# Optimization experiments

Hardware: AMD Instinct MI355X
Metric: run time of the kernel (lower is better)

Reference implementation:

```python
import jax, jax.numpy as jnp
import numpy as np
import math

FREQ = 24        # seasonality period (hours)
GAMMA = 1.0      # Matern-1/2 lengthscale (frozen in the module)
ISO = 1e-4       # global likelihood noise
TASK_NOISE = 1.0 # per-task noise (all set to 1, frozen)


def _matern12(t1, t2, ell):
    # Matern nu=0.5: k(r) = exp(-r/ell)
    return jnp.exp(-jnp.abs(t1[:, None] - t2[None, :]) / ell)


def setup_inputs() -> dict:
    key = jax.random.key(0)
    k1, k2, k3 = jax.random.split(key, 3)
    B, C, pred_len, ctx_freqs, rank = 8, 128, 24, 2, 8
    L = ctx_freqs * pred_len
    x = jax.random.normal(k1, (B, C, L), dtype=jnp.float32)
    V = jax.random.normal(k2, (C, rank), dtype=jnp.float32) * 0.3      # task covar factor
    task_var = jax.random.uniform(k3, (C,), dtype=jnp.float32) + 0.1   # task covar diag
    return {"x": x, "V": V, "task_var": task_var,
            "prediction_length": pred_len, "context_points": pred_len}


def reference(x, V, task_var, prediction_length, context_points):
    B, C, L = x.shape
    F = FREQ
    # t = arange(window_length) * pi / freq, window = context_points + prediction_length
    t = jnp.arange(context_points + prediction_length, dtype=jnp.float32) * (math.pi / F)

    # --- seasonal per-phase mean over the context (torch repeat_interleave semantics) ---
    G = L // F
    loc_phase = x[:, :, :G * F].reshape(B, C, G, F).mean(axis=2)       # [B,C,F]
    loc_ctx = jnp.repeat(loc_phase, G, axis=2)                          # [B,C,G*F]
    rem = L % F
    if rem > 0:
        loc_ctx = jnp.concatenate([loc_ctx, loc_phase[:, :, :rem]], axis=2)
    y_ctx = (x - loc_ctx).transpose(0, 2, 1)                            # [B,L,C]
    Y = y_ctx[:, L - context_points:, :]                                # [B,Lc,C] GP targets

    # --- kernels ---
    t_ctx = t[:context_points]
    t_fut = t[context_points:context_points + prediction_length]
    Kc = _matern12(t_ctx, t_ctx, GAMMA)                                 # [Lc,Lc]
    Kfc = _matern12(t_fut, t_ctx, GAMMA)                                # [Lf,Lc]
    Kff = _matern12(t_fut, t_fut, GAMMA)                                # [Lf,Lf]
    Bt = V @ V.T + jnp.diag(task_var)                                   # task covariance [C,C]
    sigma2 = TASK_NOISE + ISO                                           # isotropic noise

    # --- exact multitask GP posterior via Kronecker eigendecomposition ---
    # (Kc (x) Bt + sigma2 I)^{-1} = (U (x) P) diag(1/(s_i lam_j + sigma2)) (U (x) P)^T
    s, U = jnp.linalg.eigh(Kc)
    lam, P = jnp.linalg.eigh(Bt)
    D = s[:, None] * lam[None, :] + sigma2                               # [Lc,C]
    Yt = jnp.einsum('il,blc,cm->bim', U, Y, P)
    alpha = jnp.einsum('il,blm,cm->bic', U, Yt / D, P)                   # [B,Lc,C]
    mean_f = jnp.einsum('fi,bic,cd->bfd', Kfc, alpha, Bt)                # [B,Lf,C]

    # --- add back future seasonal mean ---
    fc, rf = divmod(prediction_length, F)
    fut_loc = jnp.repeat(loc_phase, fc, axis=2) if fc > 0 else jnp.zeros((B, C, 0), x.dtype)
    if rf > 0:
        fut_loc = jnp.concatenate([fut_loc, loc_phase[:, :, :rf]], axis=2)
    mean_final = mean_f + fut_loc.transpose(0, 2, 1)                     # [B,Lf,C]

    # --- predictive covariance of y_fut (task-interleaved: K_time (x) K_task) ---
    # shared across batch since all kernel/noise hypers are shared
    A = Kfc @ U                                                          # [Lf,Lc]
    Cm = Bt @ P                                                          # [C,C] (= P * lam)
    W = (A[:, None, :, None] * Cm[None, :, None, :]) / jnp.sqrt(D)[None, None]
    Lf = prediction_length
    W = W.reshape(Lf * C, context_points * C)
    prior = jnp.einsum('fg,cd->fcgd', Kff, Bt).reshape(Lf * C, Lf * C)
    cov = prior - W @ W.T + sigma2 * jnp.eye(Lf * C, dtype=x.dtype)      # + likelihood noise
    cov = jnp.broadcast_to(cov, (B, Lf * C, Lf * C))
    return mean_final, cov
```

## Files before the change

### kernel.cpp

```cpp
#include <hip/hip_runtime.h>
#include <math.h>

#define NB 8
#define NC 128
#define NR 8
#define NT 24
#define SIG2 1.0001f

#define OFF_KFC   0
#define OFF_KFF   576
#define OFF_U     1152
#define OFF_S     1728
#define OFF_KU    1752
#define OFF_BT    2328
#define OFF_DVEC  18712
#define OFF_VD    21784
#define OFF_INVM  46360
#define OFF_W     47896
#define OFF_J     72472
#define OFF_N     97048
#define OFF_Y     490264
#define OFF_Z     514840
#define OFF_H2    539416
#define OFF_LOCP  563992


static inline float h_fsign(float a, float b){ return copysignf(fabsf(a), b); }

static float h_slapy2(float x, float y){
  float xa=fabsf(x), ya=fabsf(y);
  float w=fmaxf(xa,ya), z=fminf(xa,ya);
  if (z==0.f) return w;
  float t=z/w;
  return w*sqrtf(1.f+t*t);
}

static void h_slartg(float f, float g, float& c, float& s, float& r){
  const float safmin=1.17549435e-38f;
  const float safmax=1.f/1.17549435e-38f;
  float f1=fabsf(f), g1=fabsf(g);
  if (g==0.f){ c=1.f; s=0.f; r=f; }
  else if (f==0.f){ c=0.f; s=copysignf(1.f,g); r=g1; }
  else {
    float rtmin=sqrtf(safmin);
    float rtmax=sqrtf(safmax*0.5f);
    if (f1>rtmin && f1<rtmax && g1>rtmin && g1<rtmax){
      float d=sqrtf(f*f+g*g);
      c=f1/d;
      r=copysignf(d,f);
      s=g/r;
    } else {
      float u=fminf(safmax, fmaxf(safmin, fmaxf(f1,g1)));
      float fs=f/u, gs=g/u;
      float d=sqrtf(fs*fs+gs*gs);
      c=fabsf(fs)/d;
      r=copysignf(d,f);
      s=gs/r;
      r=r*u;
    }
  }
}

static void h_slaev2(float a, float b, float c, float& rt1, float& rt2, float& cs1, float& sn1){
  float sm=a+c, df=a-c, adf=fabsf(df), tb=b+b, ab=fabsf(tb);
  float acmx, acmn;
  if (fabsf(a)>fabsf(c)){acmx=a;acmn=c;} else {acmx=c;acmn=a;}
  float rt;
  if (adf>ab){ float t=ab/adf; rt=adf*sqrtf(1.f+t*t); }
  else if (adf<ab){ float t=adf/ab; rt=ab*sqrtf(1.f+t*t); }
  else rt=ab*sqrtf(2.f);
  int sgn1;
  if (sm<0.f){ rt1=0.5f*(sm-rt); sgn1=-1; rt2=(acmx/rt1)*acmn-(b/rt1)*b; }
  else if (sm>0.f){ rt1=0.5f*(sm+rt); sgn1=1; rt2=(acmx/rt1)*acmn-(b/rt1)*b; }
  else { rt1=0.5f*rt; rt2=-0.5f*rt; sgn1=1; }
  float cs; int sgn2;
  if (df>=0.f){ cs=df+rt; sgn2=1; } else { cs=df-rt; sgn2=-1; }
  float acs=fabsf(cs);
  if (acs>ab){ float ct=-tb/cs; sn1=1.f/sqrtf(1.f+ct*ct); cs1=ct*sn1; }
  else {
    if (ab==0.f){ cs1=1.f; sn1=0.f; }
    else { float tn=-cs/tb; cs1=1.f/sqrtf(1.f+tn*tn); sn1=tn*cs1; }
  }
  if (sgn1==sgn2){ float tn=cs1; cs1=-sn1; sn1=tn; }
}

static void host_eigh(float* Uout , float* Sout ){
  float A[24][24], Z[24][24], dd[24], ee[24], tauv[24], wcA[24], wsA[24];
  const float h = (float)(3.14159265358979323846/24.0);
  for (int i=0;i<24;i++) for (int j=0;j<24;j++){
    float ti=(float)i*h, tj=(float)j*h;
    A[i][j]=expf(-fabsf(ti-tj));
  }
  for (int i0=0;i0<23;i0++){
    float alpha=A[i0+1][i0];
    float scale=0.f, ssq=1.f;
    for (int r=i0+2;r<24;r++){
      float ax=fabsf(A[r][i0]);
      if (ax!=0.f){
        if (scale<ax){ float t=scale/ax; ssq=1.f+ssq*t*t; scale=ax; }
        else { float t=ax/scale; ssq+=t*t; }
      }
    }
    float xnorm=scale*sqrtf(ssq);
    float taui, beta;
    if (xnorm==0.f){ taui=0.f; beta=alpha; }
    else {
      beta=-h_fsign(h_slapy2(alpha,xnorm), alpha);
      taui=(beta-alpha)/beta;
      float sc=1.f/(alpha-beta);
      for (int r=i0+2;r<24;r++) A[r][i0]*=sc;
    }
    ee[i0]=beta; tauv[i0]=taui;
    A[i0+1][i0]=1.f;
    if (taui!=0.f){
      int m=23-i0;
      float w[24];
      for (int jj=0;jj<m;jj++){
        int j=i0+1+jj;
        float acc=0.f;
        for (int k=i0+1;k<=j;k++) acc+=A[j][k]*A[k][i0];
        for (int k=j+1;k<24;k++)  acc+=A[k][j]*A[k][i0];
        w[jj]=taui*acc;
      }
      float dt=0.f;
      for (int r=0;r<m;r++) dt+=w[r]*A[i0+1+r][i0];
      float al=-0.5f*taui*dt;
      for (int r=0;r<m;r++) w[r]+=al*A[i0+1+r][i0];
      for (int jj=0;jj<m;jj++){
        int j=i0+1+jj;
        float vj=A[j][i0], wj=w[jj];
        for (int k=i0+1;k<=j;k++) A[j][k]-=vj*w[k-(i0+1)]+wj*A[k][i0];
      }
    }
    A[i0+1][i0]=ee[i0]; dd[i0]=A[i0][i0];
  }
  dd[23]=A[23][23];
  for (int i=0;i<24;i++) for (int j=0;j<24;j++) Z[i][j]=(i==j)?1.f:0.f;
  const float LEPS=5.9604645e-08f, EPS2=LEPS*LEPS, SAFMIN=1.17549435e-38f;
  const float SSFMAX=sqrtf(1.f/SAFMIN)/3.f, SSFMIN=sqrtf(SAFMIN)/EPS2;
  const int NMAXIT=720;
  #define D1(i) dd[(i)-1]
  #define E1(i) ee[(i)-1]
  #define WC1(i) wcA[(i)-1]
  #define WS1(i) wsA[(i)-1]
  int l=1,lend=1,lsv=1,lendsv=1,l1=1,jtot=0,iscale=0;
  float anorm=0.f;
  int phase=0;
  for (int guard=0; guard<200000; ++guard){
    if (phase==4) break;
    if (phase==0){
      if (l1>24){ phase=4; continue; }
      if (l1>1) E1(l1-1)=0.f;
      int m=24;
      for (int mm=l1; mm<=23; mm++){
        float tst=fabsf(E1(mm));
        if (tst==0.f){ m=mm; break; }
        if (tst<=(sqrtf(fabsf(D1(mm)))*sqrtf(fabsf(D1(mm+1))))*LEPS){ E1(mm)=0.f; m=mm; break; }
      }
      l=l1; lsv=l; lend=m; lendsv=m; l1=m+1;
      if (lend==l) continue;
      anorm=0.f;
      for (int i=l;i<=lend;i++) anorm=fmaxf(anorm,fabsf(D1(i)));
      for (int i=l;i<=lend-1;i++) anorm=fmaxf(anorm,fabsf(E1(i)));
      iscale=0;
      if (anorm==0.f) continue;
      if (anorm>SSFMAX){ iscale=1; float sc=SSFMAX/anorm; for (int i=l;i<=lend;i++) D1(i)*=sc; for (int i=l;i<lend;i++) E1(i)*=sc; }
      else if (anorm<SSFMIN){ iscale=2; float sc=SSFMIN/anorm; for (int i=l;i<=lend;i++) D1(i)*=sc; for (int i=l;i<lend;i++) E1(i)*=sc; }
      if (fabsf(D1(lend))<fabsf(D1(l))){ lend=lsv; l=lendsv; }
      phase=(lend>l)?1:2;
      continue;
    }
    if (phase==1){
      int m=lend;
      if (l!=lend){
        for (int mm=l;mm<=lend-1;mm++){
          float tst=fabsf(E1(mm)); tst*=tst;
          if (tst<=(EPS2*fabsf(D1(mm)))*fabsf(D1(mm+1))+SAFMIN){ m=mm; break; }
        }
      }
      if (m<lend) E1(m)=0.f;
      float p=D1(l);
      if (m==l){ D1(l)=p; l=l+1; if (l>lend) phase=3; continue; }
      if (m==l+1){
        float rt1,rt2,cc,ssv;
        h_slaev2(D1(l),E1(l),D1(l+1),rt1,rt2,cc,ssv);
        WC1(l)=cc; WS1(l)=ssv;
        D1(l)=rt1; D1(l+1)=rt2; E1(l)=0.f;
        for (int j=l;j>=l;j--){
          float ct=WC1(j), stv=WS1(j);
          if (ct!=1.f || stv!=0.f)
            for (int r=0;r<24;r++){ float zb=Z[r][j], za=Z[r][j-1]; Z[r][j]=ct*zb-stv*za; Z[r][j-1]=stv*zb+ct*za; }
        }
        l=l+2;
        if (l>lend) phase=3;
        continue;
      }
      if (jtot==NMAXIT){ phase=3; continue; }
      jtot++;
      float g=(D1(l+1)-p)/(2.f*E1(l));
      float r=h_slapy2(g,1.f);
      g=D1(m)-p+(E1(l)/(g+h_fsign(r,g)));
      float sv=1.f, cv=1.f;
      p=0.f;
      for (int i=m-1;i>=l;i--){
        float fv=sv*E1(i), bv=cv*E1(i);
        h_slartg(g,fv,cv,sv,r);
        if (i!=m-1) E1(i+1)=r;
        g=D1(i+1)-p;
        r=(D1(i)-g)*sv+2.f*cv*bv;
        p=sv*r;
        D1(i+1)=g+p;
        g=cv*r-bv;
        WC1(i)=cv; WS1(i)=-sv;
      }
      D1(l)=D1(l)-p;
      E1(l)=g;
      for (int j=m-1;j>=l;j--){
        float ct=WC1(j), stv=WS1(j);
        if (ct!=1.f || stv!=0.f)
          for (int r=0;r<24;r++){ float zb=Z[r][j], za=Z[r][j-1]; Z[r][j]=ct*zb-stv*za; Z[r][j-1]=stv*zb+ct*za; }
      }
      continue;
    }
    if (phase==2){
      int m=lend;
      if (l!=lend){
        for (int mm=l;mm>=lend+1;mm--){
          float tst=fabsf(E1(mm-1)); tst*=tst;
          if (tst<=(EPS2*fabsf(D1(mm)))*fabsf(D1(mm-1))+SAFMIN){ m=mm; break; }
        }
      }
      if (m>lend) E1(m-1)=0.f;
      float p=D1(l);
      if (m==l){ D1(l)=p; l=l-1; if (l<lend) phase=3; continue; }
      if (m==l-1){
        float rt1,rt2,cc,ssv;
        h_slaev2(D1(l-1),E1(l-1),D1(l),rt1,rt2,cc,ssv);
        WC1(m)=cc; WS1(m)=ssv;
        D1(l-1)=rt1; D1(l)=rt2; E1(l-1)=0.f;
        for (int j=m;j<=m;j++){
          float ct=WC1(j), stv=WS1(j);
          if (ct!=1.f || stv!=0.f)
            for (int r=0;r<24;r++){ float zb=Z[r][j], za=Z[r][j-1]; Z[r][j]=ct*zb-stv*za; Z[r][j-1]=stv*zb+ct*za; }
        }
        l=l-2;
        if (l<lend) phase=3;
        continue;
      }
      if (jtot==NMAXIT){ phase=3; continue; }
      jtot++;
      float g=(D1(l-1)-p)/(2.f*E1(l-1));
      float r=h_slapy2(g,1.f);
      g=D1(m)-p+(E1(l-1)/(g+h_fsign(r,g)));
      float sv=1.f, cv=1.f;
      p=0.f;
      for (int i=m;i<=l-1;i++){
        float fv=sv*E1(i), bv=cv*E1(i);
        h_slartg(g,fv,cv,sv,r);
        if (i!=m) E1(i-1)=r;
        g=D1(i)-p;
        r=(D1(i+1)-g)*sv+2.f*cv*bv;
        p=sv*r;
        D1(i)=g+p;
        g=cv*r-bv;
        WC1(i)=cv; WS1(i)=sv;
      }
      D1(l)=D1(l)-p;
      E1(l-1)=g;
      for (int j=m;j<=l-1;j++){
        float ct=WC1(j), stv=WS1(j);
        if (ct!=1.f || stv!=0.f)
          for (int r=0;r<24;r++){ float zb=Z[r][j], za=Z[r][j-1]; Z[r][j]=ct*zb-stv*za; Z[r][j-1]=stv*zb+ct*za; }
      }
      continue;
    }
    if (phase==3){
      if (iscale==1){ float sc=anorm/SSFMAX; for (int i=lsv;i<=lendsv;i++) D1(i)*=sc; for (int i=lsv;i<lendsv;i++) E1(i)*=sc; }
      else if (iscale==2){ float sc=anorm/SSFMIN; for (int i=lsv;i<=lendsv;i++) D1(i)*=sc; for (int i=lsv;i<lendsv;i++) E1(i)*=sc; }
      phase=(jtot<NMAXIT)?0:4;
      continue;
    }
  }
  for (int ii=2; ii<=24; ii++){
    int i=ii-1, k=i; float p=D1(i);
    for (int jq=ii;jq<=24;jq++) if (D1(jq)<p){ k=jq; p=D1(jq); }
    if (k!=i){
      D1(k)=D1(i); D1(i)=p;
      for (int r=0;r<24;r++){ float t=Z[r][i-1]; Z[r][i-1]=Z[r][k-1]; Z[r][k-1]=t; }
    }
  }
  #undef D1
  #undef E1
  #undef WC1
  #undef WS1
  for (int jc=0;jc<24;jc++){
    for (int i0=22;i0>=0;i0--){
      float taui=tauv[i0];
      if (taui!=0.f){
        float wv=Z[i0+1][jc];
        for (int r=i0+2;r<24;r++) wv+=A[r][i0]*Z[r][jc];
        Z[i0+1][jc]-=taui*wv;
        for (int r=i0+2;r<24;r++) Z[r][jc]-=taui*A[r][i0]*wv;
      }
    }
  }
  for (int i=0;i<24;i++) for (int j=0;j<24;j++) Uout[i*24+j]=Z[i][j];
  for (int i=0;i<24;i++) Sout[i]=dd[i];
}


struct EigPack { float u[576]; float s[24]; };

__global__ __launch_bounds__(256) void k1b_const(EigPack p, float* __restrict__ ws){
  int tid=threadIdx.x;
  __shared__ float Ush[24][24], Kfsh[24][24];
  const float h = (float)(3.14159265358979323846/24.0);
  for (int idx=tid; idx<576; idx+=256){
    int i=idx/24, j=idx%24;
    float u=p.u[idx];
    Ush[i][j]=u;
    ws[OFF_U+idx]=u;
    float tf=(float)(24+i)*h, tj=(float)j*h, tg=(float)(24+j)*h;
    float kfc=expf(-fabsf(tf-tj));
    Kfsh[i][j]=kfc;
    ws[OFF_KFC+idx]=kfc;
    ws[OFF_KFF+idx]=expf(-fabsf(tf-tg));
  }
  if (tid<24) ws[OFF_S+tid]=p.s[tid];
  __syncthreads();
  for (int idx=tid; idx<576; idx+=256){
    int f=idx/24, lq=idx%24;
    float acc=0.f;
    for (int i=0;i<24;i++) acc+=Kfsh[f][i]*Ush[i][lq];
    ws[OFF_KU+idx]=acc;
  }
}

__global__ __launch_bounds__(256) void k0_bt(const float* __restrict__ V, const float* __restrict__ tv, float* __restrict__ ws){
  int idx=blockIdx.x*256+threadIdx.x;
  int c=idx>>7, d=idx&127;
  float acc=0.f;
  for (int r=0;r<8;r++) acc+=V[c*8+r]*V[d*8+r];
  if (c==d) acc+=tv[c];
  ws[OFF_BT+idx]=acc;
}

__global__ __launch_bounds__(256) void k4_y(const float* __restrict__ x, float* __restrict__ ws){
  int idx=blockIdx.x*256+threadIdx.x;
  int b=idx/3072, r2=idx%3072, i=r2/128, j=r2&127;
  const float* xb=x+(size_t)(b*128+j)*48;
  ws[OFF_Y + b*3072 + i*128 + j] = xb[24+i]-0.5f*(xb[12+(i>>1)]+xb[36+(i>>1)]);
  ws[OFF_LOCP + (b*128+j)*24 + i] = 0.5f*(xb[i]+xb[24+i]);
}

__global__ __launch_bounds__(128) void k2_wood(const float* __restrict__ V, const float* __restrict__ tv, float* __restrict__ ws){
  int l=blockIdx.x, c=threadIdx.x;
  __shared__ float Msh[8][8], invMsh[8][8];
  float sl=ws[OFF_S+l];
  float dv=1.f/(sl*tv[c]+SIG2);
  ws[OFF_DVEC+l*128+c]=dv;
  for (int r=0;r<8;r++) ws[OFF_VD+(l*128+c)*8+r]=dv*V[c*8+r];
  __syncthreads();
  if (c<64){
    int r1=c>>3, r2=c&7;
    float a=0.f;
    for (int k=0;k<128;k++) a+=V[k*8+r1]*ws[OFF_VD+(l*128+k)*8+r2];
    Msh[r1][r2]=((r1==r2)?1.f:0.f)+sl*a;
  }
  __syncthreads();
  float accw[8]={0,0,0,0,0,0,0,0};
  for (int k=0;k<128;k++){
    float btck=ws[OFF_BT+c*128+k];
    const float* vdk=ws+OFF_VD+(l*128+k)*8;
    for (int r=0;r<8;r++) accw[r]+=btck*vdk[r];
  }
  for (int r=0;r<8;r++) ws[OFF_W+(l*128+c)*8+r]=accw[r];
  __syncthreads();
  if (c==0){
    float a[8][16];
    for (int i=0;i<8;i++) for (int j=0;j<8;j++){ a[i][j]=Msh[i][j]; a[i][8+j]=(i==j)?1.f:0.f; }
    for (int col=0;col<8;col++){
      int piv=col; float mx=fabsf(a[col][col]);
      for (int r2=col+1;r2<8;r2++){ float v2=fabsf(a[r2][col]); if (v2>mx){mx=v2;piv=r2;} }
      if (piv!=col) for (int j=0;j<16;j++){ float t=a[col][j]; a[col][j]=a[piv][j]; a[piv][j]=t; }
      float dinv=1.f/a[col][col];
      for (int j=0;j<16;j++) a[col][j]*=dinv;
      for (int r2=0;r2<8;r2++) if (r2!=col){
        float fq=a[r2][col];
        for (int j=0;j<16;j++) a[r2][j]-=fq*a[col][j];
      }
    }
    for (int i=0;i<8;i++) for (int j=0;j<8;j++) invMsh[i][j]=a[i][8+j];
  }
  __syncthreads();
  if (c<64) ws[OFF_INVM+l*64+c]=invMsh[c>>3][c&7];
  for (int q=0;q<8;q++){
    float accj=0.f;
    for (int r=0;r<8;r++) accj+=accw[r]*invMsh[r][q];
    ws[OFF_J+(l*128+c)*8+q]=accj;
  }
}

__global__ __launch_bounds__(256) void k3_n(float* __restrict__ ws){
  int l=blockIdx.x;
  int idx=blockIdx.y*256+threadIdx.x;
  int c=idx>>7, e=idx&127;
  float sl=ws[OFF_S+l];
  const float* btc=ws+OFF_BT+c*128;
  const float* dv=ws+OFF_DVEC+l*128;
  float acc=0.f;
  for (int k=0;k<128;k++) acc+=btc[k]*dv[k]*ws[OFF_BT+k*128+e];
  float acc2=0.f;
  const float* jc=ws+OFF_J+(l*128+c)*8;
  const float* we=ws+OFF_W+(l*128+e)*8;
  for (int r=0;r<8;r++) acc2+=jc[r]*we[r];
  ws[OFF_N+l*16384+idx]=acc-sl*acc2;
}

__global__ __launch_bounds__(256) void k5_z(float* __restrict__ ws){
  int idx=blockIdx.x*256+threadIdx.x;
  int b=idx/3072, r2=idx%3072, l=r2/128, c=r2&127;
  const float* Urow=ws+OFF_U+l*24;
  float acc=0.f;
  for (int k=0;k<24;k++) acc+=Urow[k]*ws[OFF_Y+b*3072+k*128+c];
  ws[OFF_Z+idx]=acc;
}

__global__ __launch_bounds__(128) void k6_h(float* __restrict__ ws){
  int b=blockIdx.x/24, l=blockIdx.x%24, c=threadIdx.x;
  __shared__ float zsh[128], wsh[128], u8[8], y8[8];
  float sl=ws[OFF_S+l];
  zsh[c]=ws[OFF_Z+b*3072+l*128+c];
  __syncthreads();
  if (c<8){ float a=0.f; for (int k=0;k<128;k++) a+=ws[OFF_VD+(l*128+k)*8+c]*zsh[k]; u8[c]=a; }
  __syncthreads();
  if (c<8){ float a=0.f; for (int r=0;r<8;r++) a+=ws[OFF_INVM+l*64+c*8+r]*u8[r]; y8[c]=a; }
  __syncthreads();
  {
    float a=0.f;
    const float* vdc=ws+OFF_VD+(l*128+c)*8;
    for (int r=0;r<8;r++) a+=vdc[r]*y8[r];
    wsh[c]=ws[OFF_DVEC+l*128+c]*zsh[c]-sl*a;
  }
  __syncthreads();
  float acc=0.f;
  for (int k=0;k<128;k++) acc+=wsh[k]*ws[OFF_BT+k*128+c];
  ws[OFF_H2+b*3072+l*128+c]=acc;
}

__global__ __launch_bounds__(256) void k7_mean(const float* __restrict__ ws, float* __restrict__ out){
  int idx=blockIdx.x*256+threadIdx.x;
  int b=idx/3072, r2=idx%3072, f=r2/128, c=r2&127;
  float acc=0.f;
  for (int l=0;l<24;l++) acc+=ws[OFF_KU+f*24+l]*ws[OFF_H2+b*3072+l*128+c];
  out[idx]=acc+ws[OFF_LOCP+(b*128+c)*24+f];
}

__global__ __launch_bounds__(256) void k8_cov(const float* __restrict__ ws, float* __restrict__ cov){
  int f=blockIdx.x, tile=blockIdx.y, tid=threadIdx.x;
  __shared__ float wfg[576], kffr[24];
  for (int idx=tid; idx<576; idx+=256){
    int g=idx/24, i=idx%24;
    wfg[idx]=ws[OFF_KU+f*24+i]*ws[OFF_KU+g*24+i];
  }
  if (tid<24) kffr[tid]=ws[OFF_KFF+f*24+tid];
  __syncthreads();
  int cd4=tile*256+tid;
  int c=cd4>>5, d0=(cd4&31)*4;
  float4 Nv[24];
  #pragma unroll
  for (int i=0;i<24;i++) Nv[i]=*(const float4*)(ws+OFF_N+i*16384+c*128+d0);
  float4 btv=*(const float4*)(ws+OFF_BT+c*128+d0);
  long rowbase=(long)(f*128+c)*3072;
  for (int g=0;g<24;g++){
    float ax=0.f,ay=0.f,az=0.f,aw=0.f;
    #pragma unroll
    for (int i=0;i<24;i++){
      float w=wfg[g*24+i];
      ax+=w*Nv[i].x; ay+=w*Nv[i].y; az+=w*Nv[i].z; aw+=w*Nv[i].w;
    }
    float kf=kffr[g];
    float4 val;
    val.x=kf*btv.x-ax; val.y=kf*btv.y-ay; val.z=kf*btv.z-az; val.w=kf*btv.w-aw;
    if (g==f && c>=d0 && c<d0+4){
      if (c==d0) val.x+=SIG2; else if (c==d0+1) val.y+=SIG2; else if (c==d0+2) val.z+=SIG2; else val.w+=SIG2;
    }
    long off=rowbase+g*128+d0;
    #pragma unroll
    for (int b=0;b<8;b++){
      *(float4*)(cov+off+(long)b*9437184)=val;
    }
  }
}

extern "C" void kernel_launch(void* const* d_in, const int* in_sizes, int n_in,
                              void* d_out, int out_size, void* d_ws, size_t ws_size,
                              hipStream_t stream){
  (void)in_sizes; (void)n_in; (void)out_size; (void)ws_size;
  const float* x  = (const float*)d_in[0];
  const float* V  = (const float*)d_in[1];
  const float* tv = (const float*)d_in[2];
  float* out = (float*)d_out;
  float* ws  = (float*)d_ws;
  float* cov = out + 24576;

  EigPack pack;
  host_eigh(pack.u, pack.s);

  k1b_const<<<1,256,0,stream>>>(pack,ws);
  k0_bt<<<64,256,0,stream>>>(V,tv,ws);
  k4_y<<<96,256,0,stream>>>(x,ws);
  k2_wood<<<24,128,0,stream>>>(V,tv,ws);
  k3_n<<<dim3(24,64),256,0,stream>>>(ws);
  k5_z<<<96,256,0,stream>>>(ws);
  k6_h<<<192,128,0,stream>>>(ws);
  k7_mean<<<96,256,0,stream>>>(ws,out);
  k8_cov<<<dim3(24,16),256,0,stream>>>(ws,cov);
}
```

Before: 433.1 us.

## Fuse setup and mean-path kernels to cut launches and workspace traffic

Merges the Bt and constant-setup kernels into one launch and keeps the Woodbury intermediates in shared memory across 256 threads. The separate y, z, h and mean kernels become a single per-batch kernel that holds Bt, U and the residuals in shared memory and loops over eigen-indices. This removes several launches and global round-trips. In exchange the mean path now runs on only 8 blocks with a serial loop of many barriers, and the large shared-memory footprint limits occupancy.

```diff
diff --git a/kernel.cpp b/kernel.cpp
--- a/kernel.cpp
+++ b/kernel.cpp
@@ -311,8 +311,20 @@
 
 struct EigPack { float u[576]; float s[24]; };
 
-__global__ __launch_bounds__(256) void k1b_const(EigPack p, float* __restrict__ ws){
+__global__ __launch_bounds__(256) void ka_setup(EigPack p,
+                                                const float* __restrict__ V,
+                                                const float* __restrict__ tv,
+                                                float* __restrict__ ws){
   int tid=threadIdx.x;
+  if (blockIdx.x < 64){
+    int idx=blockIdx.x*256+tid;
+    int c=idx>>7, d=idx&127;
+    float acc=0.f;
+    for (int r=0;r<8;r++) acc+=V[c*8+r]*V[d*8+r];
+    if (c==d) acc+=tv[c];
+    ws[OFF_BT+idx]=acc;
+    return;
+  }
   __shared__ float Ush[24][24], Kfsh[24][24];
   const float h = (float)(3.14159265358979323846/24.0);
   for (int idx=tid; idx<576; idx+=256){
@@ -321,9 +333,7 @@
     Ush[i][j]=u;
     ws[OFF_U+idx]=u;
     float tf=(float)(24+i)*h, tj=(float)j*h, tg=(float)(24+j)*h;
-    float kfc=expf(-fabsf(tf-tj));
-    Kfsh[i][j]=kfc;
-    ws[OFF_KFC+idx]=kfc;
+    Kfsh[i][j]=expf(-fabsf(tf-tj));
     ws[OFF_KFF+idx]=expf(-fabsf(tf-tg));
   }
   if (tid<24) ws[OFF_S+tid]=p.s[tid];
@@ -336,47 +346,26 @@
   }
 }
 
-__global__ __launch_bounds__(256) void k0_bt(const float* __restrict__ V, const float* __restrict__ tv, float* __restrict__ ws){
-  int idx=blockIdx.x*256+threadIdx.x;
-  int c=idx>>7, d=idx&127;
-  float acc=0.f;
-  for (int r=0;r<8;r++) acc+=V[c*8+r]*V[d*8+r];
-  if (c==d) acc+=tv[c];
-  ws[OFF_BT+idx]=acc;
-}
-
-__global__ __launch_bounds__(256) void k4_y(const float* __restrict__ x, float* __restrict__ ws){
-  int idx=blockIdx.x*256+threadIdx.x;
-  int b=idx/3072, r2=idx%3072, i=r2/128, j=r2&127;
-  const float* xb=x+(size_t)(b*128+j)*48;
-  ws[OFF_Y + b*3072 + i*128 + j] = xb[24+i]-0.5f*(xb[12+(i>>1)]+xb[36+(i>>1)]);
-  ws[OFF_LOCP + (b*128+j)*24 + i] = 0.5f*(xb[i]+xb[24+i]);
-}
-
-__global__ __launch_bounds__(128) void k2_wood(const float* __restrict__ V, const float* __restrict__ tv, float* __restrict__ ws){
-  int l=blockIdx.x, c=threadIdx.x;
-  __shared__ float Msh[8][8], invMsh[8][8];
+__global__ __launch_bounds__(256) void kb1_wood(const float* __restrict__ V,
+                                                const float* __restrict__ tv,
+                                                float* __restrict__ ws){
+  int l=blockIdx.x, tid=threadIdx.x;
+  __shared__ float Vdsh[128][8], Wsh[128][8], Msh[8][8], invMsh[8][8];
   float sl=ws[OFF_S+l];
-  float dv=1.f/(sl*tv[c]+SIG2);
-  ws[OFF_DVEC+l*128+c]=dv;
-  for (int r=0;r<8;r++) ws[OFF_VD+(l*128+c)*8+r]=dv*V[c*8+r];
-  __syncthreads();
-  if (c<64){
-    int r1=c>>3, r2=c&7;
+  if (tid<128){
+    float dv=1.f/(sl*tv[tid]+SIG2);
+    ws[OFF_DVEC+l*128+tid]=dv;
+    for (int r=0;r<8;r++) Vdsh[tid][r]=dv*V[tid*8+r];
+  }
+  __syncthreads();
+  if (tid<64){
+    int r1=tid>>3, r2=tid&7;
     float a=0.f;
-    for (int k=0;k<128;k++) a+=V[k*8+r1]*ws[OFF_VD+(l*128+k)*8+r2];
+    for (int k=0;k<128;k++) a+=V[k*8+r1]*Vdsh[k][r2];
     Msh[r1][r2]=((r1==r2)?1.f:0.f)+sl*a;
   }
   __syncthreads();
-  float accw[8]={0,0,0,0,0,0,0,0};
-  for (int k=0;k<128;k++){
-    float btck=ws[OFF_BT+c*128+k];
-    const float* vdk=ws+OFF_VD+(l*128+k)*8;
-    for (int r=0;r<8;r++) accw[r]+=btck*vdk[r];
-  }
-  for (int r=0;r<8;r++) ws[OFF_W+(l*128+c)*8+r]=accw[r];
-  __syncthreads();
-  if (c==0){
+  if (tid==0){
     float a[8][16];
     for (int i=0;i<8;i++) for (int j=0;j<8;j++){ a[i][j]=Msh[i][j]; a[i][8+j]=(i==j)?1.f:0.f; }
     for (int col=0;col<8;col++){
@@ -393,11 +382,31 @@
     for (int i=0;i<8;i++) for (int j=0;j<8;j++) invMsh[i][j]=a[i][8+j];
   }
   __syncthreads();
-  if (c<64) ws[OFF_INVM+l*64+c]=invMsh[c>>3][c&7];
-  for (int q=0;q<8;q++){
-    float accj=0.f;
-    for (int r=0;r<8;r++) accj+=accw[r]*invMsh[r][q];
-    ws[OFF_J+(l*128+c)*8+q]=accj;
+  if (tid<64) ws[OFF_INVM+l*64+tid]=invMsh[tid>>3][tid&7];
+  {
+    int hh=tid>>7, c=tid&127;
+    float acc[4]={0.f,0.f,0.f,0.f};
+    const float* btc=ws+OFF_BT+c*128;
+    for (int k=0;k<128;k++){
+      float btck=btc[k];
+      #pragma unroll
+      for (int q=0;q<4;q++) acc[q]+=btck*Vdsh[k][4*hh+q];
+    }
+    #pragma unroll
+    for (int q=0;q<4;q++){
+      Wsh[c][4*hh+q]=acc[q];
+      ws[OFF_W+(l*128+c)*8+4*hh+q]=acc[q];
+    }
+  }
+  __syncthreads();
+  {
+    int hh=tid>>7, c=tid&127;
+    #pragma unroll
+    for (int q=0;q<4;q++){
+      float a=0.f;
+      for (int r=0;r<8;r++) a+=Wsh[c][r]*invMsh[r][4*hh+q];
+      ws[OFF_J+(l*128+c)*8+4*hh+q]=a;
+    }
   }
 }
 
@@ -417,43 +426,96 @@
   ws[OFF_N+l*16384+idx]=acc-sl*acc2;
 }
 
-__global__ __launch_bounds__(256) void k5_z(float* __restrict__ ws){
-  int idx=blockIdx.x*256+threadIdx.x;
-  int b=idx/3072, r2=idx%3072, l=r2/128, c=r2&127;
-  const float* Urow=ws+OFF_U+l*24;
-  float acc=0.f;
-  for (int k=0;k<24;k++) acc+=Urow[k]*ws[OFF_Y+b*3072+k*128+c];
-  ws[OFF_Z+idx]=acc;
-}
-
-__global__ __launch_bounds__(128) void k6_h(float* __restrict__ ws){
-  int b=blockIdx.x/24, l=blockIdx.x%24, c=threadIdx.x;
-  __shared__ float zsh[128], wsh[128], u8[8], y8[8];
-  float sl=ws[OFF_S+l];
-  zsh[c]=ws[OFF_Z+b*3072+l*128+c];
-  __syncthreads();
-  if (c<8){ float a=0.f; for (int k=0;k<128;k++) a+=ws[OFF_VD+(l*128+k)*8+c]*zsh[k]; u8[c]=a; }
-  __syncthreads();
-  if (c<8){ float a=0.f; for (int r=0;r<8;r++) a+=ws[OFF_INVM+l*64+c*8+r]*u8[r]; y8[c]=a; }
-  __syncthreads();
-  {
-    float a=0.f;
-    const float* vdc=ws+OFF_VD+(l*128+c)*8;
-    for (int r=0;r<8;r++) a+=vdc[r]*y8[r];
-    wsh[c]=ws[OFF_DVEC+l*128+c]*zsh[c]-sl*a;
-  }
-  __syncthreads();
-  float acc=0.f;
-  for (int k=0;k<128;k++) acc+=wsh[k]*ws[OFF_BT+k*128+c];
-  ws[OFF_H2+b*3072+l*128+c]=acc;
-}
-
-__global__ __launch_bounds__(256) void k7_mean(const float* __restrict__ ws, float* __restrict__ out){
-  int idx=blockIdx.x*256+threadIdx.x;
-  int b=idx/3072, r2=idx%3072, f=r2/128, c=r2&127;
-  float acc=0.f;
-  for (int l=0;l<24;l++) acc+=ws[OFF_KU+f*24+l]*ws[OFF_H2+b*3072+l*128+c];
-  out[idx]=acc+ws[OFF_LOCP+(b*128+c)*24+f];
+__global__ __launch_bounds__(256) void kd_mean(const float* __restrict__ x,
+                                               const float* __restrict__ V,
+                                               const float* __restrict__ tv,
+                                               const float* __restrict__ ws,
+                                               float* __restrict__ out){
+  __shared__ float Btsh[128][128];
+  __shared__ float Ysh[24][128];
+  __shared__ float Zsh[24][128];
+  __shared__ float Vsh[128][8];
+  __shared__ float tvsh[128];
+  __shared__ float Ush[576], KUsh[576], Ssh[24];
+  __shared__ float u8sh[8], y8sh[8], wsh[128], H2sh[128];
+  int b=blockIdx.x, tid=threadIdx.x;
+  for (int i=tid;i<4096;i+=256)
+    ((float4*)&Btsh[0][0])[i] = ((const float4*)(ws+OFF_BT))[i];
+  for (int i=tid;i<576;i+=256){ Ush[i]=ws[OFF_U+i]; KUsh[i]=ws[OFF_KU+i]; }
+  if (tid<24) Ssh[tid]=ws[OFF_S+tid];
+  if (tid<128){
+    tvsh[tid]=tv[tid];
+    for (int r=0;r<8;r++) Vsh[tid][r]=V[tid*8+r];
+  }
+  for (int idx=tid; idx<3072; idx+=256){
+    int i=idx>>7, j=idx&127;
+    const float* xb=x+(size_t)(b*128+j)*48;
+    Ysh[i][j]=xb[24+i]-0.5f*(xb[12+(i>>1)]+xb[36+(i>>1)]);
+  }
+  __syncthreads();
+  for (int idx=tid; idx<3072; idx+=256){
+    int l=idx>>7, c=idx&127;
+    float acc=0.f;
+    for (int k=0;k<24;k++) acc+=Ush[l*24+k]*Ysh[k][c];
+    Zsh[l][c]=acc;
+  }
+  float mf[12];
+  #pragma unroll
+  for (int j=0;j<12;j++) mf[j]=0.f;
+  __syncthreads();
+  for (int l=0;l<24;l++){
+    float sl=Ssh[l];
+    {
+      int r=tid>>5, lane=tid&31;
+      float part=0.f;
+      for (int c=lane;c<128;c+=32){
+        float dv=1.f/(sl*tvsh[c]+SIG2);
+        part+=dv*Vsh[c][r]*Zsh[l][c];
+      }
+      part+=__shfl_xor(part,16);
+      part+=__shfl_xor(part,8);
+      part+=__shfl_xor(part,4);
+      part+=__shfl_xor(part,2);
+      part+=__shfl_xor(part,1);
+      if (lane==0) u8sh[r]=part;
+    }
+    __syncthreads();
+    if (tid<8){
+      float a=0.f;
+      for (int r=0;r<8;r++) a+=ws[OFF_INVM+l*64+tid*8+r]*u8sh[r];
+      y8sh[tid]=a;
+    }
+    __syncthreads();
+    if (tid<128){
+      int c=tid;
+      float dv=1.f/(sl*tvsh[c]+SIG2);
+      float vd=0.f;
+      #pragma unroll
+      for (int r=0;r<8;r++) vd+=dv*Vsh[c][r]*y8sh[r];
+      wsh[c]=dv*Zsh[l][c]-sl*vd;
+    }
+    __syncthreads();
+    if (tid<128){
+      int c=tid;
+      float acc=0.f;
+      for (int k=0;k<128;k++) acc+=wsh[k]*Btsh[k][c];
+      H2sh[c]=acc;
+    }
+    __syncthreads();
+    #pragma unroll
+    for (int j=0;j<12;j++){
+      int idx=tid+j*256;
+      mf[j]+=KUsh[(idx>>7)*24+l]*H2sh[idx&127];
+    }
+    __syncthreads();
+  }
+  #pragma unroll
+  for (int j=0;j<12;j++){
+    int idx=tid+j*256;
+    int f=idx>>7, c=idx&127;
+    const float* xb=x+(size_t)(b*128+c)*48;
+    out[b*3072+idx]=mf[j]+0.5f*(xb[f]+xb[24+f]);
+  }
 }
 
 __global__ __launch_bounds__(256) void k8_cov(const float* __restrict__ ws, float* __restrict__ cov){
@@ -507,13 +569,9 @@
   EigPack pack;
   host_eigh(pack.u, pack.s);
 
-  k1b_const<<<1,256,0,stream>>>(pack,ws);
-  k0_bt<<<64,256,0,stream>>>(V,tv,ws);
-  k4_y<<<96,256,0,stream>>>(x,ws);
-  k2_wood<<<24,128,0,stream>>>(V,tv,ws);
+  ka_setup<<<65,256,0,stream>>>(pack,V,tv,ws);
+  kb1_wood<<<24,256,0,stream>>>(V,tv,ws);
   k3_n<<<dim3(24,64),256,0,stream>>>(ws);
-  k5_z<<<96,256,0,stream>>>(ws);
-  k6_h<<<192,128,0,stream>>>(ws);
-  k7_mean<<<96,256,0,stream>>>(ws,out);
+  kd_mean<<<8,256,0,stream>>>(x,V,tv,ws,out);
   k8_cov<<<dim3(24,16),256,0,stream>>>(ws,cov);
 }
```

After: 475.8 us. +9.8%, slower.
